# Kernel tuning notes

Hardware: AMD Instinct MI355X
Metric: run time of the kernel (lower is better)

## Reference

```python
import jax, jax.numpy as jnp
import numpy as np

LEAK_RATE = 0.9
SPECTRAL_RADIUS = 0.95


def setup_inputs() -> dict:
    key = jax.random.key(0)
    k1, k2, k3, k4, k5 = jax.random.split(key, 5)
    B, T, R, F, I = 8, 4096, 1024, 64, 32
    feedback = jax.random.normal(k1, (B, T, F), dtype=jnp.float32)
    driving = jax.random.normal(k2, (B, T, I), dtype=jnp.float32)
    # default init: uniform(-1, 1) for all weight matrices
    W_fb = jax.random.uniform(k3, (R, F), minval=-1.0, maxval=1.0, dtype=jnp.float32)
    W_in = jax.random.uniform(k4, (R, I), minval=-1.0, maxval=1.0, dtype=jnp.float32)
    W_hh = jax.random.uniform(k5, (R, R), minval=-1.0, maxval=1.0, dtype=jnp.float32)
    # scale recurrent weights to target spectral radius (done once at init, like torch)
    eig = np.linalg.eigvals(np.asarray(W_hh))
    rho = float(np.max(np.abs(eig)))
    W_hh = jnp.asarray(np.asarray(W_hh) * (SPECTRAL_RADIUS / rho), dtype=jnp.float32)
    b = jnp.zeros((R,), dtype=jnp.float32)
    return {"feedback": feedback, "driving": driving, "W_fb": W_fb, "W_in": W_in, "W_hh": W_hh, "b": b}


def reference(feedback, driving, W_fb, W_in, W_hh, b):
    # Precompute the input-driven projection for all timesteps in one big GEMM: [B,T,R]
    drive = jnp.einsum("btf,rf->btr", feedback, W_fb) + jnp.einsum("bti,ri->btr", driving, W_in) + b
    B, T, R = drive.shape
    alpha = jnp.asarray(LEAK_RATE, drive.dtype)

    def step(h, u_t):
        # pre-activation: W_fb x_fb + W_in x_in + b (precomputed) + W_rec h_{t-1}
        pre = u_t + h @ W_hh.T  # [B,R]
        h_new = jnp.tanh((1.0 - alpha) * h + alpha * pre)
        return h_new, h_new

    h0 = jnp.zeros((B, R), drive.dtype)
    _, states = jax.lax.scan(step, h0, jnp.swapaxes(drive, 0, 1))  # [T,B,R]
    return jnp.swapaxes(states, 0, 1)  # [B,T,R]
```

## Files before the change

### kernel.cpp

```cpp
#include <hip/hip_runtime.h>
#include <math.h>

#define TT 4096
#define RR 1024
#define FF 64
#define II 32
#define GROUPS 8
#define BPG 32
#define THREADS 256
#define KV4 32
#define ALPHA 0.9f
#define TCH 32

typedef unsigned long long u64;
typedef unsigned int u32;
typedef u32 u32x4 __attribute__((ext_vector_type(4)));

#define SLOT_U32 (GROUPS * RR)
#define CNT_BASE (2 * SLOT_U32)
#define PAD(i) ((i) + (((i) >> 7) << 2))

__device__ __forceinline__ u32x4 ld_agent16(const u32x4* p) {
    u32x4 v;
    asm volatile("global_load_dwordx4 %0, %1, off sc1\n\t"
                 "s_waitcnt vmcnt(0)"
                 : "=v"(v) : "v"(p) : "memory");
    return v;
}
__device__ __forceinline__ u32 ld_agent32(const u32* p) {
    u32 v;
    asm volatile("global_load_dword %0, %1, off sc1\n\t"
                 "s_waitcnt vmcnt(0)"
                 : "=v"(v) : "v"(p) : "memory");
    return v;
}

__device__ __forceinline__ u32x4 poll4(const u32x4* p, u32 wtag) {
    u32x4 v = ld_agent16(p);
    while ((((v[0] ^ wtag) | (v[1] ^ wtag) | (v[2] ^ wtag) | (v[3] ^ wtag)) & 1u) != 0u)
        v = ld_agent16(p);
    return v;
}

__device__ __forceinline__ void st_pub64(u64* p, u64 v) {
    (void)__hip_atomic_exchange(p, v, __ATOMIC_RELAXED, __HIP_MEMORY_SCOPE_AGENT);
}
__device__ __forceinline__ void st_pub32(u32* p, u32 v) {
    (void)__hip_atomic_exchange(p, v, __ATOMIC_RELAXED, __HIP_MEMORY_SCOPE_AGENT);
}

__device__ __forceinline__ float fast_tanh(float x) {
    float ax = fabsf(x);
    float e  = __expf(2.0f * fminf(ax, 10.0f));
    float r  = (e - 1.0f) * __builtin_amdgcn_rcpf(e + 1.0f);
    return x < 0.0f ? -r : r;
}

__global__ __launch_bounds__(256, 1)
void drive_pre(const float* __restrict__ feedback,
               const float* __restrict__ driving,
               const float* __restrict__ W_fb,
               const float* __restrict__ W_in,
               float* __restrict__ out)
{
    const int tid = threadIdx.x;
    const int b   = blockIdx.x >> 7;
    const int t0  = (blockIdx.x & 127) * TCH;

    __shared__ float xch[TCH][96];

    const float4* fb4 = (const float4*)(feedback + ((size_t)b * TT + t0) * FF);
    #pragma unroll
    for (int q = 0; q < 2; q++) {
        int i = tid + 256 * q;
        float4 v = fb4[i];
        *(float4*)&xch[i >> 4][(i & 15) << 2] = v;
    }
    {
        const float4* dr4 = (const float4*)(driving + ((size_t)b * TT + t0) * II);
        float4 v = dr4[tid];
        *(float4*)&xch[tid >> 3][64 + ((tid & 7) << 2)] = v;
    }
    __syncthreads();

    #pragma unroll 1
    for (int p = 0; p < 4; p++) {
        const int r = p * 256 + tid;
        float4 w[24];
        const float4* wf4 = (const float4*)(W_fb + (size_t)r * FF);
        #pragma unroll
        for (int q = 0; q < 16; q++) w[q] = wf4[q];
        const float4* wi4 = (const float4*)(W_in + (size_t)r * II);
        #pragma unroll
        for (int q = 0; q < 8; q++) w[16 + q] = wi4[q];

        for (int t = 0; t < TCH; t++) {
            float s = 0.0f;
            #pragma unroll
            for (int q = 0; q < 24; q++) {
                float4 x = *(const float4*)&xch[t][q << 2];
                s = fmaf(w[q].x, x.x, s);
                s = fmaf(w[q].y, x.y, s);
                s = fmaf(w[q].z, x.z, s);
                s = fmaf(w[q].w, x.w, s);
            }
            out[((size_t)b * TT + (t0 + t)) * RR + r] = s;
        }
    }
}

__global__ __launch_bounds__(THREADS, 1)
void reservoir_df(const float* __restrict__ W_hh,
                  const float* __restrict__ bias,
                  float* __restrict__ out,
                  u32* __restrict__ hbuf)
{
    const int tid  = threadIdx.x;
    const int bid  = blockIdx.x;
    const int g    = bid & 7;
    const int rank = bid >> 3;
    const int lr   = tid >> 3;
    const int j    = tid & 7;
    const int row  = rank * 32 + lr;

    float4 w4[KV4];
    {
        const float4* whh4 = (const float4*)(W_hh + (size_t)row * RR);
        #pragma unroll
        for (int i = 0; i < KV4; i++) w4[i] = whh4[j * KV4 + i];
    }
    const float brow = bias[row];

    __shared__ float hlds[2][1056];

    float* outg = out + (size_t)g * TT * RR;
    u32*       myflag   = hbuf + CNT_BASE + (g << 5) + rank;
    const u32* pollbase = hbuf + CNT_BASE + (g << 5);

    float dreg = (j == 0) ? outg[row] : 0.0f;

    for (int t = 0; t < TT; t++) {
        const int par = t & 1;

        if (t > 0 && tid < 64) {
            const u32* fp = pollbase + (tid & 31);
            u32 v = ld_agent32(fp);
            while (!__all((int)(v >= (u32)t))) v = ld_agent32(fp);
        }

        float dnext = 0.0f;
        if (j == 0 && t + 1 < TT) dnext = outg[(size_t)(t + 1) * RR + row];

        __syncthreads();

        const u32x4* sp4 = (const u32x4*)(hbuf + (size_t)par * SLOT_U32 + (size_t)g * RR) + tid;
        const u32x4 hv = poll4(sp4, (u32)((t >> 1) & 1));
        const float f0 = __uint_as_float(hv[0]);
        const float f1 = __uint_as_float(hv[1]);
        const float f2 = __uint_as_float(hv[2]);
        const float f3 = __uint_as_float(hv[3]);

        if (t > 0 && lr == rank) {
            *(float4*)(outg + (size_t)(t - 1) * RR + 4 * tid) = make_float4(f0, f1, f2, f3);
        }

        *(float4*)&hlds[par][PAD(4 * tid)] = make_float4(f0, f1, f2, f3);

        __syncthreads();

        float4 acc = make_float4(0.f, 0.f, 0.f, 0.f);
        const float* hb = &hlds[par][j * 132];
        #pragma unroll
        for (int i = 0; i < KV4; i++) {
            float4 hvv = *(const float4*)(hb + 4 * i);
            acc.x = fmaf(w4[i].x, hvv.x, acc.x);
            acc.y = fmaf(w4[i].y, hvv.y, acc.y);
            acc.z = fmaf(w4[i].z, hvv.z, acc.z);
            acc.w = fmaf(w4[i].w, hvv.w, acc.w);
        }

        float s = (acc.x + acc.y) + (acc.z + acc.w);
        s += __shfl_xor(s, 1, 64);
        s += __shfl_xor(s, 2, 64);
        s += __shfl_xor(s, 4, 64);

        u32 bits = 0u;
        if (j == 0) {
            const float hold = hlds[par][PAD(row)];
            const float pre  = (1.0f - ALPHA) * hold + ALPHA * (s + dreg + brow);
            const float hnew = fast_tanh(pre);
            bits = (__float_as_uint(hnew) & ~1u) | (u32)(((t + 1) >> 1) & 1);
            dreg = dnext;
        }
        const u32 partner = __shfl_xor(bits, 8, 64);
        if ((tid & 15) == 0) {
            u64* dst = (u64*)(hbuf + (size_t)((t + 1) & 1) * SLOT_U32 + (size_t)g * RR + row);
            st_pub64(dst, (u64)bits | ((u64)partner << 32));
        }

        asm volatile("s_barrier" ::: "memory");

        if (tid == 64) st_pub32(myflag, (u32)(t + 1));
    }

    if (lr == rank) {
        const u32x4* sp4 = (const u32x4*)(hbuf + (size_t)g * RR) + tid;
        const u32x4 hv = poll4(sp4, 0u);
        *(float4*)(outg + (size_t)(TT - 1) * RR + 4 * tid) =
            make_float4(__uint_as_float(hv[0]), __uint_as_float(hv[1]),
                        __uint_as_float(hv[2]), __uint_as_float(hv[3]));
    }
}

extern "C" void kernel_launch(void* const* d_in, const int* in_sizes, int n_in,
                              void* d_out, int out_size, void* d_ws, size_t ws_size,
                              hipStream_t stream) {
    const float* feedback = (const float*)d_in[0];
    const float* driving  = (const float*)d_in[1];
    const float* W_fb     = (const float*)d_in[2];
    const float* W_in     = (const float*)d_in[3];
    const float* W_hh     = (const float*)d_in[4];
    const float* bias     = (const float*)d_in[5];
    float* out = (float*)d_out;

    u32* hbuf = (u32*)d_ws;
    hipMemsetAsync(d_ws, 0x00, SLOT_U32 * sizeof(u32), stream);
    hipMemsetAsync((char*)d_ws + SLOT_U32 * sizeof(u32), 0x01, SLOT_U32 * sizeof(u32), stream);
    hipMemsetAsync((char*)d_ws + 2 * SLOT_U32 * sizeof(u32), 0x00, 16 * 64, stream);

    hipLaunchKernelGGL(drive_pre, dim3(GROUPS * (TT / TCH)), dim3(256), 0, stream,
                       feedback, driving, W_fb, W_in, out);

    void* args[] = { (void*)&W_hh, (void*)&bias, (void*)&out, (void*)&hbuf };
    hipError_t ce = hipLaunchCooperativeKernel((const void*)reservoir_df,
                                               dim3(GROUPS * BPG), dim3(THREADS), args, 0, stream);
    if (ce != hipSuccess) {
        hipLaunchKernelGGL(reservoir_df, dim3(GROUPS * BPG), dim3(THREADS), 0, stream,
                           W_hh, bias, out, hbuf);
    }
}
```

Baseline: 7.882 ms.

## Process two batch groups per block with shared register-resident W_hh slice

Each persistent block now serves two batch groups instead of one, halving the grid from 256 to 128 blocks. The block keeps its W_hh row slice in registers and runs the poll, matvec and publish sequence for each group in turn within a timestep. This makes each W_hh slice do double duty and lets the groups' synchronisation latencies interleave. In exchange the per-step critical path per block is serialised across two groups, and each group's flag wait now sits behind the other group's work.

```diff
diff --git a/kernel.cpp b/kernel.cpp
--- a/kernel.cpp
+++ b/kernel.cpp
@@ -7,6 +7,8 @@
 #define II 32
 #define GROUPS 8
 #define BPG 32
+#define GPB 2
+#define NBLK (BPG * GROUPS / GPB)
 #define THREADS 256
 #define KV4 32
 #define ALPHA 0.9f
@@ -117,8 +119,8 @@
 {
     const int tid  = threadIdx.x;
     const int bid  = blockIdx.x;
-    const int g    = bid & 7;
-    const int rank = bid >> 3;
+    const int gp   = bid & 3;
+    const int rank = bid >> 2;
     const int lr   = tid >> 3;
     const int j    = tid & 7;
     const int row  = rank * 32 + lr;
@@ -131,84 +133,101 @@
     }
     const float brow = bias[row];
 
-    __shared__ float hlds[2][1056];
-
-    float* outg = out + (size_t)g * TT * RR;
-    u32*       myflag   = hbuf + CNT_BASE + (g << 5) + rank;
-    const u32* pollbase = hbuf + CNT_BASE + (g << 5);
-
-    float dreg = (j == 0) ? outg[row] : 0.0f;
+    __shared__ float hlds[GPB][2][1056];
+
+    float*     outg[GPB];
+    u32*       myflag[GPB];
+    const u32* pollbase[GPB];
+    float      dreg[GPB];
+    #pragma unroll
+    for (int gi = 0; gi < GPB; gi++) {
+        const int g  = gp * GPB + gi;
+        outg[gi]     = out + (size_t)g * TT * RR;
+        myflag[gi]   = hbuf + CNT_BASE + (g << 5) + rank;
+        pollbase[gi] = hbuf + CNT_BASE + (g << 5);
+        dreg[gi]     = (j == 0) ? outg[gi][row] : 0.0f;
+    }
 
     for (int t = 0; t < TT; t++) {
         const int par = t & 1;
 
-        if (t > 0 && tid < 64) {
-            const u32* fp = pollbase + (tid & 31);
-            u32 v = ld_agent32(fp);
-            while (!__all((int)(v >= (u32)t))) v = ld_agent32(fp);
+        #pragma unroll
+        for (int gi = 0; gi < GPB; gi++) {
+            const int g = gp * GPB + gi;
+
+            if (t > 0 && tid < 64) {
+                const u32* fp = pollbase[gi] + (tid & 31);
+                u32 v = ld_agent32(fp);
+                while (!__all((int)(v >= (u32)t))) v = ld_agent32(fp);
+            }
+
+            float dnext = 0.0f;
+            if (j == 0 && t + 1 < TT) dnext = outg[gi][(size_t)(t + 1) * RR + row];
+
+            __syncthreads();
+
+            const u32x4* sp4 = (const u32x4*)(hbuf + (size_t)par * SLOT_U32 + (size_t)g * RR) + tid;
+            const u32x4 hv = poll4(sp4, (u32)((t >> 1) & 1));
+            const float f0 = __uint_as_float(hv[0]);
+            const float f1 = __uint_as_float(hv[1]);
+            const float f2 = __uint_as_float(hv[2]);
+            const float f3 = __uint_as_float(hv[3]);
+
+            if (t > 0 && lr == rank) {
+                *(float4*)(outg[gi] + (size_t)(t - 1) * RR + 4 * tid) =
+                    make_float4(f0, f1, f2, f3);
+            }
+
+            *(float4*)&hlds[gi][par][PAD(4 * tid)] = make_float4(f0, f1, f2, f3);
+
+            __syncthreads();
+
+            float4 acc = make_float4(0.f, 0.f, 0.f, 0.f);
+            const float* hb = &hlds[gi][par][j * 132];
+            #pragma unroll
+            for (int i = 0; i < KV4; i++) {
+                float4 hvv = *(const float4*)(hb + 4 * i);
+                acc.x = fmaf(w4[i].x, hvv.x, acc.x);
+                acc.y = fmaf(w4[i].y, hvv.y, acc.y);
+                acc.z = fmaf(w4[i].z, hvv.z, acc.z);
+                acc.w = fmaf(w4[i].w, hvv.w, acc.w);
+            }
+
+            float s = (acc.x + acc.y) + (acc.z + acc.w);
+            s += __shfl_xor(s, 1, 64);
+            s += __shfl_xor(s, 2, 64);
+            s += __shfl_xor(s, 4, 64);
+
+            u32 bits = 0u;
+            if (j == 0) {
+                const float hold = hlds[gi][par][PAD(row)];
+                const float pre  = (1.0f - ALPHA) * hold + ALPHA * (s + dreg[gi] + brow);
+                const float hnew = fast_tanh(pre);
+                bits = (__float_as_uint(hnew) & ~1u) | (u32)(((t + 1) >> 1) & 1);
+                dreg[gi] = dnext;
+            }
+            const u32 partner = __shfl_xor(bits, 8, 64);
+            if ((tid & 15) == 0) {
+                u64* dst = (u64*)(hbuf + (size_t)((t + 1) & 1) * SLOT_U32 + (size_t)g * RR + row);
+                st_pub64(dst, (u64)bits | ((u64)partner << 32));
+            }
+
+            asm volatile("s_barrier" ::: "memory");
+
+            if (tid == 64) st_pub32(myflag[gi], (u32)(t + 1));
         }
-
-        float dnext = 0.0f;
-        if (j == 0 && t + 1 < TT) dnext = outg[(size_t)(t + 1) * RR + row];
-
-        __syncthreads();
-
-        const u32x4* sp4 = (const u32x4*)(hbuf + (size_t)par * SLOT_U32 + (size_t)g * RR) + tid;
-        const u32x4 hv = poll4(sp4, (u32)((t >> 1) & 1));
-        const float f0 = __uint_as_float(hv[0]);
-        const float f1 = __uint_as_float(hv[1]);
-        const float f2 = __uint_as_float(hv[2]);
-        const float f3 = __uint_as_float(hv[3]);
-
-        if (t > 0 && lr == rank) {
-            *(float4*)(outg + (size_t)(t - 1) * RR + 4 * tid) = make_float4(f0, f1, f2, f3);
+    }
+
+    if (lr == rank) {
+        #pragma unroll
+        for (int gi = 0; gi < GPB; gi++) {
+            const int g = gp * GPB + gi;
+            const u32x4* sp4 = (const u32x4*)(hbuf + (size_t)g * RR) + tid;
+            const u32x4 hv = poll4(sp4, 0u);
+            *(float4*)(outg[gi] + (size_t)(TT - 1) * RR + 4 * tid) =
+                make_float4(__uint_as_float(hv[0]), __uint_as_float(hv[1]),
+                            __uint_as_float(hv[2]), __uint_as_float(hv[3]));
         }
-
-        *(float4*)&hlds[par][PAD(4 * tid)] = make_float4(f0, f1, f2, f3);
-
-        __syncthreads();
-
-        float4 acc = make_float4(0.f, 0.f, 0.f, 0.f);
-        const float* hb = &hlds[par][j * 132];
-        #pragma unroll
-        for (int i = 0; i < KV4; i++) {
-            float4 hvv = *(const float4*)(hb + 4 * i);
-            acc.x = fmaf(w4[i].x, hvv.x, acc.x);
-            acc.y = fmaf(w4[i].y, hvv.y, acc.y);
-            acc.z = fmaf(w4[i].z, hvv.z, acc.z);
-            acc.w = fmaf(w4[i].w, hvv.w, acc.w);
-        }
-
-        float s = (acc.x + acc.y) + (acc.z + acc.w);
-        s += __shfl_xor(s, 1, 64);
-        s += __shfl_xor(s, 2, 64);
-        s += __shfl_xor(s, 4, 64);
-
-        u32 bits = 0u;
-        if (j == 0) {
-            const float hold = hlds[par][PAD(row)];
-            const float pre  = (1.0f - ALPHA) * hold + ALPHA * (s + dreg + brow);
-            const float hnew = fast_tanh(pre);
-            bits = (__float_as_uint(hnew) & ~1u) | (u32)(((t + 1) >> 1) & 1);
-            dreg = dnext;
-        }
-        const u32 partner = __shfl_xor(bits, 8, 64);
-        if ((tid & 15) == 0) {
-            u64* dst = (u64*)(hbuf + (size_t)((t + 1) & 1) * SLOT_U32 + (size_t)g * RR + row);
-            st_pub64(dst, (u64)bits | ((u64)partner << 32));
-        }
-
-        asm volatile("s_barrier" ::: "memory");
-
-        if (tid == 64) st_pub32(myflag, (u32)(t + 1));
-    }
-
-    if (lr == rank) {
-        const u32x4* sp4 = (const u32x4*)(hbuf + (size_t)g * RR) + tid;
-        const u32x4 hv = poll4(sp4, 0u);
-        *(float4*)(outg + (size_t)(TT - 1) * RR + 4 * tid) =
-            make_float4(__uint_as_float(hv[0]), __uint_as_float(hv[1]),
-                        __uint_as_float(hv[2]), __uint_as_float(hv[3]));
     }
 }
 
@@ -233,9 +252,9 @@
 
     void* args[] = { (void*)&W_hh, (void*)&bias, (void*)&out, (void*)&hbuf };
     hipError_t ce = hipLaunchCooperativeKernel((const void*)reservoir_df,
-                                               dim3(GROUPS * BPG), dim3(THREADS), args, 0, stream);
+                                               dim3(NBLK), dim3(THREADS), args, 0, stream);
     if (ce != hipSuccess) {
-        hipLaunchKernelGGL(reservoir_df, dim3(GROUPS * BPG), dim3(THREADS), 0, stream,
+        hipLaunchKernelGGL(reservoir_df, dim3(NBLK), dim3(THREADS), 0, stream,
                            W_hh, bias, out, hbuf);
     }
 }
```

Measured after the change: 13.49 ms. 71.1% more time.
